# Kernel tuning notes

Measured on AMD Instinct MI355X. Metric: run time of the kernel, lower is better.

Reference implementation:

```python
import jax, jax.numpy as jnp
import numpy as np

B, LQ, D, H, L, P, DFF = 16, 1024, 256, 8, 4, 4, 1024
SHAPES = ((64, 64), (32, 32), (16, 16), (8, 8))  # (H_l, W_l) per level
LV = sum(h * w for h, w in SHAPES)  # 5440
DH = D // H
EPS = 1e-5


def layer_norm(x, g, b):
    m = jnp.mean(x, -1, keepdims=True)
    v = jnp.mean((x - m) ** 2, -1, keepdims=True)
    return (x - m) * jax.lax.rsqrt(v + EPS) * g + b


def mha(q_in, k_in, v_in, w, b, ow, ob):
    # torch nn.MultiheadAttention with packed in_proj [3D, D]
    q = (q_in @ w[:D].T + b[:D]).reshape(B, LQ, H, DH)
    k = (k_in @ w[D:2 * D].T + b[D:2 * D]).reshape(B, LQ, H, DH)
    v = (v_in @ w[2 * D:].T + b[2 * D:]).reshape(B, LQ, H, DH)
    a = jax.nn.softmax(jnp.einsum('bqhd,bkhd->bhqk', q, k) * (1.0 / np.sqrt(DH)), -1)
    o = jnp.einsum('bhqk,bkhd->bqhd', a, v).reshape(B, LQ, D)
    return o @ ow.T + ob


def ms_deform_attn(q, ref, src, value_w, value_b, off_w, off_b, attw_w, attw_b, outp_w, outp_b):
    # value: [B, H, LV, DH]
    value = (src @ value_w.T + value_b).reshape(B, LV, H, DH).transpose(0, 2, 1, 3)
    off = (q @ off_w.T + off_b).reshape(B, LQ, H, L, P, 2)
    attw = jax.nn.softmax((q @ attw_w.T + attw_b).reshape(B, LQ, H, L * P), -1).reshape(B, LQ, H, L, P)
    # offset normalizer = (W_l, H_l) matching (x, y) order of reference points
    normalizer = jnp.array([[w, h] for h, w in SHAPES], jnp.float32)
    loc = ref[:, :, None, :, None, :] + off / normalizer[None, None, None, :, None, :]  # [B,LQ,H,L,P,2]
    out = jnp.zeros((B, LQ, H, DH), jnp.float32)
    start = 0
    for l, (hl, wl) in enumerate(SHAPES):
        v = value[:, :, start:start + hl * wl]  # [B,H,N_l,DH]
        start += hl * wl
        # grid_sample semantics, align_corners=False, padding zeros
        x = loc[:, :, :, l, :, 0] * wl - 0.5  # [B,LQ,H,P]
        y = loc[:, :, :, l, :, 1] * hl - 0.5
        x0 = jnp.floor(x); y0 = jnp.floor(y)
        lx = (x - x0).transpose(0, 2, 1, 3)[..., None]  # [B,H,LQ,P,1]
        ly = (y - y0).transpose(0, 2, 1, 3)[..., None]
        x0i = x0.astype(jnp.int32); y0i = y0.astype(jnp.int32)

        def gather(xi, yi):
            valid = ((xi >= 0) & (xi < wl) & (yi >= 0) & (yi < hl)).astype(jnp.float32)
            idx = jnp.clip(yi, 0, hl - 1) * wl + jnp.clip(xi, 0, wl - 1)  # [B,LQ,H,P]
            idx2 = idx.transpose(0, 2, 1, 3).reshape(B, H, LQ * P)
            g = jnp.take_along_axis(v, jnp.broadcast_to(idx2[..., None], (B, H, LQ * P, DH)), axis=2)
            return g.reshape(B, H, LQ, P, DH) * valid.transpose(0, 2, 1, 3)[..., None]

        g00 = gather(x0i, y0i); g01 = gather(x0i + 1, y0i)
        g10 = gather(x0i, y0i + 1); g11 = gather(x0i + 1, y0i + 1)
        sampled = (g00 * (1 - lx) * (1 - ly) + g01 * lx * (1 - ly)
                   + g10 * (1 - lx) * ly + g11 * lx * ly)  # [B,H,LQ,P,DH]
        out = out + jnp.einsum('bhqpd,bqhp->bqhd', sampled, attw[:, :, :, l])
    return out.reshape(B, LQ, D) @ outp_w.T + outp_b


def setup_inputs() -> dict:
    key = jax.random.key(0)
    ks = jax.random.split(key, 16)
    s = 0.02
    inp = {}
    inp['tgt'] = jax.random.normal(ks[0], (B, LQ, D), jnp.float32)
    inp['query_pos'] = jax.random.normal(ks[1], (B, LQ, D), jnp.float32)
    inp['reference_points'] = jax.random.uniform(ks[2], (B, LQ, L, 2), jnp.float32)
    inp['src'] = jax.random.normal(ks[3], (B, LV, D), jnp.float32)
    # self-attention (MHA)
    inp['in_proj_w'] = jax.random.normal(ks[4], (3 * D, D), jnp.float32) * s
    inp['in_proj_b'] = jnp.zeros((3 * D,), jnp.float32)
    inp['out_proj_w'] = jax.random.normal(ks[5], (D, D), jnp.float32) * s
    inp['out_proj_b'] = jnp.zeros((D,), jnp.float32)
    inp['norm2_g'] = jnp.ones((D,), jnp.float32); inp['norm2_b'] = jnp.zeros((D,), jnp.float32)
    # MSDeformAttn
    inp['value_w'] = jax.random.normal(ks[6], (D, D), jnp.float32) * s
    inp['value_b'] = jnp.zeros((D,), jnp.float32)
    inp['off_w'] = jax.random.normal(ks[7], (H * L * P * 2, D), jnp.float32) * s
    inp['off_b'] = jax.random.normal(ks[8], (H * L * P * 2,), jnp.float32) * 0.5
    inp['attw_w'] = jax.random.normal(ks[9], (H * L * P, D), jnp.float32) * s
    inp['attw_b'] = jnp.zeros((H * L * P,), jnp.float32)
    inp['outp_w'] = jax.random.normal(ks[10], (D, D), jnp.float32) * s
    inp['outp_b'] = jnp.zeros((D,), jnp.float32)
    inp['norm1_g'] = jnp.ones((D,), jnp.float32); inp['norm1_b'] = jnp.zeros((D,), jnp.float32)
    # FFN
    inp['lin1_w'] = jax.random.normal(ks[11], (DFF, D), jnp.float32) * s
    inp['lin1_b'] = jnp.zeros((DFF,), jnp.float32)
    inp['lin2_w'] = jax.random.normal(ks[12], (D, DFF), jnp.float32) * s
    inp['lin2_b'] = jnp.zeros((D,), jnp.float32)
    inp['norm3_g'] = jnp.ones((D,), jnp.float32); inp['norm3_b'] = jnp.zeros((D,), jnp.float32)
    inp['src_spatial_shapes'] = jnp.array(SHAPES, jnp.int32)
    inp['level_start_index'] = jnp.array(np.concatenate([[0], np.cumsum([h * w for h, w in SHAPES[:-1]])]), jnp.int32)
    return inp


def reference(tgt, query_pos, reference_points, src,
              in_proj_w, in_proj_b, out_proj_w, out_proj_b, norm2_g, norm2_b,
              value_w, value_b, off_w, off_b, attw_w, attw_b, outp_w, outp_b,
              norm1_g, norm1_b, lin1_w, lin1_b, lin2_w, lin2_b, norm3_g, norm3_b,
              src_spatial_shapes, level_start_index):
    # dropout=0 (eval mode)
    q = tgt + query_pos
    tgt2 = mha(q, q, tgt, in_proj_w, in_proj_b, out_proj_w, out_proj_b)
    tgt = layer_norm(tgt + tgt2, norm2_g, norm2_b)
    tgt2 = ms_deform_attn(tgt + query_pos, reference_points, src,
                          value_w, value_b, off_w, off_b, attw_w, attw_b, outp_w, outp_b)
    tgt = layer_norm(tgt + tgt2, norm1_g, norm1_b)
    t2 = jax.nn.relu(tgt @ lin1_w.T + lin1_b) @ lin2_w.T + lin2_b
    return layer_norm(tgt + t2, norm3_g, norm3_b)
```

## Files before the change

### kernel.cpp

```cpp
#include <hip/hip_runtime.h>
#include <math.h>

typedef short s16x8 __attribute__((ext_vector_type(8)));
typedef float f32x4 __attribute__((ext_vector_type(4)));
typedef unsigned short u16;
typedef unsigned short u16x4 __attribute__((ext_vector_type(4)));

constexpr int cB    = 16;
constexpr int cLQ   = 1024;
constexpr int cD    = 256;
constexpr int cH    = 8;
constexpr int cLVTOT= 5440;
constexpr int cNTOK = cB * cLQ;
constexpr int cNV   = cB * cLVTOT;

__device__ __forceinline__ u16 f2b(float f) {
    __bf16 h = (__bf16)f;
    u16 u;
    __builtin_memcpy(&u, &h, 2);
    return u;
}
__device__ __forceinline__ float bl(unsigned x) {
    return __uint_as_float(x << 16);
}
__device__ __forceinline__ void load16(const u16* g, u16* l) {
    __builtin_amdgcn_global_load_lds((const __attribute__((address_space(1))) void*)g,
                                     (__attribute__((address_space(3))) void*)l, 16, 0, 0);
}

__global__ __launch_bounds__(256) void cvt_kernel(const float4* __restrict__ in,
                                                  u16x4* __restrict__ out) {
    int i = blockIdx.x * 256 + threadIdx.x;
    float4 v = in[i];
    out[i] = (u16x4){ f2b(v.x), f2b(v.y), f2b(v.z), f2b(v.w) };
}

struct WArgs { const float4* src[8]; };
__global__ __launch_bounds__(256) void cvtw_kernel(WArgs a, u16x4* __restrict__ out) {
    int i = blockIdx.x * 256 + threadIdx.x;
    int s, off;
    if (i < 98304) {
        if (i < 65536) { if (i < 49152) { s = 0; off = i; } else { s = 1; off = i - 49152; } }
        else           { if (i < 81920) { s = 2; off = i - 65536; } else { s = 3; off = i - 81920; } }
    } else {
        if (i < 122880){ if (i < 106496){ s = 4; off = i - 98304; } else { s = 5; off = i - 106496; } }
        else           { if (i < 188416){ s = 6; off = i - 122880; } else { s = 7; off = i - 188416; } }
    }
    float4 v = a.src[s][off];
    out[i] = (u16x4){ f2b(v.x), f2b(v.y), f2b(v.z), f2b(v.w) };
}

__global__ __launch_bounds__(256) void prep_kernel(const float4* __restrict__ t,
                                                   const float4* __restrict__ q,
                                                   u16x4* __restrict__ tb,
                                                   u16x4* __restrict__ qb) {
    int i = blockIdx.x * 256 + threadIdx.x;
    float4 a = t[i], b = q[i];
    tb[i] = (u16x4){ f2b(a.x), f2b(a.y), f2b(a.z), f2b(a.w) };
    qb[i] = (u16x4){ f2b(a.x + b.x), f2b(a.y + b.y), f2b(a.z + b.z), f2b(a.w + b.w) };
}

template <int RELU, int OUTBF>
__global__ __launch_bounds__(256) void gemm128(const u16* __restrict__ A,
                                               const u16* __restrict__ Wt,
                                               const float* __restrict__ bias,
                                               float* __restrict__ Cf,
                                               u16* __restrict__ Cb,
                                               int M, int N, int K) {
    __shared__ u16 As[128 * 32];
    __shared__ u16 Bs[128 * 32];
    int tid = threadIdx.x;
    int bm = blockIdx.x * 128, bn = blockIdx.y * 128;
    int w = tid >> 6, lane = tid & 63, quad = lane >> 4, l15 = lane & 15;
    int wm = (w & 1) * 64, wn = (w >> 1) * 64;
    int r0 = tid >> 2;
    int c0 = ((tid & 3) ^ ((tid >> 3) & 3)) * 8;
    const u16* ga0 = A  + (size_t)(bm + r0) * K + c0;
    const u16* ga1 = ga0 + (size_t)64 * K;
    const u16* gb0 = Wt + (size_t)(bn + r0) * K + c0;
    const u16* gb1 = gb0 + (size_t)64 * K;
    u16* la0 = As + (tid & 192) * 8;
    u16* la1 = As + 64 * 32 + (tid & 192) * 8;
    u16* lb0 = Bs + (tid & 192) * 8;
    u16* lb1 = Bs + 64 * 32 + (tid & 192) * 8;
    int abk = (quad ^ ((l15 >> 1) & 3)) * 8;
    f32x4 acc[16];
#pragma unroll
    for (int i = 0; i < 16; ++i) acc[i] = (f32x4){0.f, 0.f, 0.f, 0.f};
    for (int k0 = 0; k0 < K; k0 += 32) {
        __syncthreads();
        load16(ga0 + k0, la0);
        load16(ga1 + k0, la1);
        load16(gb0 + k0, lb0);
        load16(gb1 + k0, lb1);
        __syncthreads();
        s16x8 af[4], bf[4];
#pragma unroll
        for (int mt = 0; mt < 4; ++mt) af[mt] = *(const s16x8*)&As[(wm + mt * 16 + l15) * 32 + abk];
#pragma unroll
        for (int nt = 0; nt < 4; ++nt) bf[nt] = *(const s16x8*)&Bs[(wn + nt * 16 + l15) * 32 + abk];
#pragma unroll
        for (int mt = 0; mt < 4; ++mt)
#pragma unroll
            for (int nt = 0; nt < 4; ++nt)
                acc[mt * 4 + nt] = __builtin_amdgcn_mfma_f32_16x16x32_bf16(af[mt], bf[nt], acc[mt * 4 + nt], 0, 0, 0);
    }
    float bs[4];
#pragma unroll
    for (int nt = 0; nt < 4; ++nt) bs[nt] = bias[bn + wn + nt * 16 + l15];
#pragma unroll
    for (int mt = 0; mt < 4; ++mt) {
        int m = bm + wm + mt * 16 + quad * 4;
#pragma unroll
        for (int nt = 0; nt < 4; ++nt) {
            int n = bn + wn + nt * 16 + l15;
#pragma unroll
            for (int r = 0; r < 4; ++r) {
                float v = acc[mt * 4 + nt][r] + bs[nt];
                if (RELU) v = fmaxf(v, 0.f);
                if (OUTBF) Cb[(size_t)(m + r) * N + n] = f2b(v);
                else       Cf[(size_t)(m + r) * N + n] = v;
            }
        }
    }
}

template <int RELU, int OUTBF>
__global__ __launch_bounds__(256) void gemm64(const u16* __restrict__ A,
                                              const u16* __restrict__ Wt,
                                              const float* __restrict__ bias,
                                              float* __restrict__ Cf,
                                              u16* __restrict__ Cb,
                                              int M, int N, int K) {
    __shared__ u16 As[64 * 32];
    __shared__ u16 Bs[128 * 32];
    int tid = threadIdx.x;
    int bm = blockIdx.x * 64, bn = blockIdx.y * 128;
    int w = tid >> 6, lane = tid & 63, quad = lane >> 4, l15 = lane & 15;
    int wn = w * 32;
    int r0 = tid >> 2;
    int c0 = ((tid & 3) ^ ((tid >> 3) & 3)) * 8;
    const u16* ga0 = A  + (size_t)(bm + r0) * K + c0;
    const u16* gb0 = Wt + (size_t)(bn + r0) * K + c0;
    const u16* gb1 = gb0 + (size_t)64 * K;
    u16* la0 = As + (tid & 192) * 8;
    u16* lb0 = Bs + (tid & 192) * 8;
    u16* lb1 = Bs + 64 * 32 + (tid & 192) * 8;
    int abk = (quad ^ ((l15 >> 1) & 3)) * 8;
    f32x4 acc[8];
#pragma unroll
    for (int i = 0; i < 8; ++i) acc[i] = (f32x4){0.f, 0.f, 0.f, 0.f};
    for (int k0 = 0; k0 < K; k0 += 32) {
        __syncthreads();
        load16(ga0 + k0, la0);
        load16(gb0 + k0, lb0);
        load16(gb1 + k0, lb1);
        __syncthreads();
        s16x8 af[4], bf[2];
#pragma unroll
        for (int mt = 0; mt < 4; ++mt) af[mt] = *(const s16x8*)&As[(mt * 16 + l15) * 32 + abk];
#pragma unroll
        for (int nt = 0; nt < 2; ++nt) bf[nt] = *(const s16x8*)&Bs[(wn + nt * 16 + l15) * 32 + abk];
#pragma unroll
        for (int mt = 0; mt < 4; ++mt)
#pragma unroll
            for (int nt = 0; nt < 2; ++nt)
                acc[mt * 2 + nt] = __builtin_amdgcn_mfma_f32_16x16x32_bf16(af[mt], bf[nt], acc[mt * 2 + nt], 0, 0, 0);
    }
    float bs[2];
#pragma unroll
    for (int nt = 0; nt < 2; ++nt) bs[nt] = bias[bn + wn + nt * 16 + l15];
#pragma unroll
    for (int mt = 0; mt < 4; ++mt) {
        int m = bm + mt * 16 + quad * 4;
#pragma unroll
        for (int nt = 0; nt < 2; ++nt) {
            int n = bn + wn + nt * 16 + l15;
#pragma unroll
            for (int r = 0; r < 4; ++r) {
                float v = acc[mt * 2 + nt][r] + bs[nt];
                if (RELU) v = fmaxf(v, 0.f);
                if (OUTBF) Cb[(size_t)(m + r) * N + n] = f2b(v);
                else       Cf[(size_t)(m + r) * N + n] = v;
            }
        }
    }
}

__global__ __launch_bounds__(256) void vtrans_kernel(const u16* __restrict__ Vb,
                                                     u16* __restrict__ Vtg) {
    __shared__ u16 T[64 * 40];
    int tid = threadIdx.x;
    int tt = blockIdx.x & 15, bh = blockIdx.x >> 4;
    int h = bh & 7, b = bh >> 3;
    int r = tid >> 2, c = (tid & 3) * 8;
    *(s16x8*)&T[r * 40 + c] =
        *(const s16x8*)(Vb + (size_t)(b * cLQ + tt * 64 + r) * cD + h * 32 + c);
    __syncthreads();
    int dh = tid & 31, tc = (tid >> 5) * 8;
    s16x8 o;
#pragma unroll
    for (int i = 0; i < 8; ++i) o[i] = T[(tc + i) * 40 + dh];
    *(s16x8*)(Vtg + ((size_t)bh * 32 + dh) * cLQ + tt * 64 + tc) = o;
}

__global__ __launch_bounds__(256) void attn_mfma(const u16* __restrict__ QK,
                                                 const u16* __restrict__ Vt,
                                                 u16* __restrict__ O) {
    __shared__ u16 Ks[64 * 40];
    __shared__ u16 Vs[32 * 88];
    __shared__ u16 Ps[4][16 * 88];
    int tid = threadIdx.x, w = tid >> 6, lane = tid & 63, quad = lane >> 4, l15 = lane & 15;
    int qt = blockIdx.x & 15, bh = blockIdx.x >> 4;
    int h = bh & 7, b = bh >> 3;
    int qbase = qt * 64 + w * 16;
    const float C = 0.25506734f;
    s16x8 qf = *(const s16x8*)(QK + (size_t)(b * cLQ + qbase + l15) * 512 + h * 32 + quad * 8);
    f32x4 o0 = {0.f,0.f,0.f,0.f}, o1 = {0.f,0.f,0.f,0.f};
    float lsum = 0.f;
    int skey = tid >> 2, sdh = (tid & 3) * 8;
    int vdh = tid >> 3, vkc = (tid & 7) * 8;
    size_t kgbase = (size_t)(b * cLQ) * 512 + 256 + h * 32;
    size_t vgbase = (size_t)bh * 32 * cLQ;
    for (int kt = 0; kt < cLQ; kt += 64) {
        __syncthreads();
        *(s16x8*)&Ks[skey * 40 + sdh] = *(const s16x8*)(QK + kgbase + (size_t)(kt + skey) * 512 + sdh);
        *(s16x8*)&Vs[vdh * 88 + vkc]  = *(const s16x8*)(Vt + vgbase + (size_t)vdh * cLQ + kt + vkc);
        __syncthreads();
#pragma unroll
        for (int t = 0; t < 4; ++t) {
            s16x8 kf = *(const s16x8*)&Ks[(t * 16 + l15) * 40 + quad * 8];
            f32x4 z = {0.f,0.f,0.f,0.f};
            f32x4 sc = __builtin_amdgcn_mfma_f32_16x16x32_bf16(kf, qf, z, 0, 0, 0);
            u16x4 pb;
#pragma unroll
            for (int r = 0; r < 4; ++r) {
                float p = exp2f(sc[r] * C);
                lsum += p;
                pb[r] = f2b(p);
            }
            *(u16x4*)&Ps[w][l15 * 88 + t * 16 + quad * 4] = pb;
        }
#pragma unroll
        for (int ks = 0; ks < 2; ++ks) {
            s16x8 pa  = *(const s16x8*)&Ps[w][l15 * 88 + ks * 32 + quad * 8];
            s16x8 vb0 = *(const s16x8*)&Vs[l15 * 88 + ks * 32 + quad * 8];
            s16x8 vb1 = *(const s16x8*)&Vs[(l15 + 16) * 88 + ks * 32 + quad * 8];
            o0 = __builtin_amdgcn_mfma_f32_16x16x32_bf16(pa, vb0, o0, 0, 0, 0);
            o1 = __builtin_amdgcn_mfma_f32_16x16x32_bf16(pa, vb1, o1, 0, 0, 0);
        }
    }
    lsum += __shfl_xor(lsum, 16);
    lsum += __shfl_xor(lsum, 32);
#pragma unroll
    for (int r = 0; r < 4; ++r) {
        float inv = 1.0f / __shfl(lsum, quad * 4 + r);
        int q = qbase + quad * 4 + r;
        size_t ob = (size_t)(b * cLQ + q) * cD + h * 32;
        O[ob + l15]      = f2b(o0[r] * inv);
        O[ob + 16 + l15] = f2b(o1[r] * inv);
    }
}

template <int WB, int QP>
__global__ __launch_bounds__(256) void add_ln_kernel(const float* __restrict__ X,
                                                     const float* __restrict__ R,
                                                     const float* __restrict__ g,
                                                     const float* __restrict__ bt,
                                                     const float* __restrict__ qp,
                                                     float* __restrict__ out,
                                                     u16* __restrict__ outb) {
    int wave = threadIdx.x / 64;
    int lane = threadIdx.x % 64;
    int row = blockIdx.x * 4 + wave;
    const float* x = X + (size_t)row * cD;
    const float* r = R + (size_t)row * cD;
    float4 xv = *(const float4*)(x + lane * 4);
    float4 rv = *(const float4*)(r + lane * 4);
    float v0 = xv.x + rv.x, v1 = xv.y + rv.y, v2 = xv.z + rv.z, v3 = xv.w + rv.w;
    float s = v0 + v1 + v2 + v3;
    float s2 = v0 * v0 + v1 * v1 + v2 * v2 + v3 * v3;
#pragma unroll
    for (int off = 32; off > 0; off >>= 1) {
        s += __shfl_xor(s, off);
        s2 += __shfl_xor(s2, off);
    }
    float mean = s * (1.0f / 256.0f);
    float var = s2 * (1.0f / 256.0f) - mean * mean;
    float rstd = rsqrtf(var + 1e-5f);
    float4 gv = *(const float4*)(g + lane * 4);
    float4 bv = *(const float4*)(bt + lane * 4);
    float4 o;
    o.x = (v0 - mean) * rstd * gv.x + bv.x;
    o.y = (v1 - mean) * rstd * gv.y + bv.y;
    o.z = (v2 - mean) * rstd * gv.z + bv.z;
    o.w = (v3 - mean) * rstd * gv.w + bv.w;
    *(float4*)(out + (size_t)row * cD + lane * 4) = o;
    if (WB) {
        u16x4 ob = { f2b(o.x), f2b(o.y), f2b(o.z), f2b(o.w) };
        *(u16x4*)(outb + (size_t)row * cD + lane * 4) = ob;
    }
    if (QP) {
        float4 qv = *(const float4*)(qp + (size_t)row * cD + lane * 4);
        u16x4 ob = { f2b(o.x + qv.x), f2b(o.y + qv.y), f2b(o.z + qv.z), f2b(o.w + qv.w) };
        *(u16x4*)(outb + (size_t)row * cD + lane * 4) = ob;
    }
}

__global__ __launch_bounds__(256) void deform_kernel(const u16* __restrict__ value,
                                                     const float* __restrict__ oa,
                                                     const float* __restrict__ refp,
                                                     u16* __restrict__ out) {
    int t = blockIdx.x * 32 + (threadIdx.x >> 3);
    int dq = threadIdx.x & 7;
    int h = t & 7;
    int bq = t >> 3;
    int b = bq >> 10;
    const float* al = oa + (size_t)bq * 384 + 256 + h * 16;
    float wv[16];
    float mx = -1e30f;
#pragma unroll
    for (int i = 0; i < 16; ++i) { wv[i] = al[i]; mx = fmaxf(mx, wv[i]); }
    float sum = 0.f;
#pragma unroll
    for (int i = 0; i < 16; ++i) { wv[i] = __expf(wv[i] - mx); sum += wv[i]; }
    float inv = 1.f / sum;
    const float* off = oa + (size_t)bq * 384 + h * 32;
    const float* rp = refp + (size_t)bq * 8;
    const u16* vb = value + ((size_t)b * cLVTOT) * 256 + h * 32 + dq * 4;
    const int starts[4] = {0, 4096, 5120, 5376};
    const int dims[4] = {64, 32, 16, 8};
    float a0 = 0.f, a1 = 0.f, a2 = 0.f, a3 = 0.f;
#pragma unroll
    for (int l = 0; l < 4; ++l) {
        int hl = dims[l], wl = dims[l];
        float rx = rp[l * 2 + 0], ry = rp[l * 2 + 1];
#pragma unroll
        for (int p = 0; p < 4; ++p) {
            float ox = off[(l * 4 + p) * 2 + 0];
            float oy = off[(l * 4 + p) * 2 + 1];
            float x = rx * (float)wl + ox - 0.5f;
            float y = ry * (float)hl + oy - 0.5f;
            float x0f = floorf(x), y0f = floorf(y);
            float lx = x - x0f, ly = y - y0f;
            int x0 = (int)x0f, y0 = (int)y0f;
            float aw = wv[l * 4 + p] * inv;
            float cw[4] = {(1.f - lx) * (1.f - ly), lx * (1.f - ly),
                           (1.f - lx) * ly, lx * ly};
            int xs[4] = {x0, x0 + 1, x0, x0 + 1};
            int ys[4] = {y0, y0, y0 + 1, y0 + 1};
#pragma unroll
            for (int c = 0; c < 4; ++c) {
                int xi = xs[c], yi = ys[c];
                bool valid = (xi >= 0) && (xi < wl) && (yi >= 0) && (yi < hl);
                int xc = min(max(xi, 0), wl - 1);
                int yc = min(max(yi, 0), hl - 1);
                int idx = starts[l] + yc * wl + xc;
                float wgt = valid ? aw * cw[c] : 0.f;
                unsigned long long u = *(const unsigned long long*)(vb + (size_t)idx * 256);
                a0 += wgt * bl((unsigned)(u & 0xffffull));
                a1 += wgt * bl((unsigned)((u >> 16) & 0xffffull));
                a2 += wgt * bl((unsigned)((u >> 32) & 0xffffull));
                a3 += wgt * bl((unsigned)(u >> 48));
            }
        }
    }
    u16x4 o = { f2b(a0), f2b(a1), f2b(a2), f2b(a3) };
    *(u16x4*)(out + (size_t)bq * 256 + h * 32 + dq * 4) = o;
}

extern "C" void kernel_launch(void* const* d_in, const int* in_sizes, int n_in,
                              void* d_out, int out_size, void* d_ws, size_t ws_size,
                              hipStream_t stream) {
    const float* tgt        = (const float*)d_in[0];
    const float* query_pos  = (const float*)d_in[1];
    const float* refp       = (const float*)d_in[2];
    const float* src        = (const float*)d_in[3];
    const float* in_proj_w  = (const float*)d_in[4];
    const float* in_proj_b  = (const float*)d_in[5];
    const float* out_proj_w = (const float*)d_in[6];
    const float* out_proj_b = (const float*)d_in[7];
    const float* norm2_g    = (const float*)d_in[8];
    const float* norm2_b    = (const float*)d_in[9];
    const float* value_w    = (const float*)d_in[10];
    const float* value_b    = (const float*)d_in[11];
    const float* off_w      = (const float*)d_in[12];
    const float* off_b      = (const float*)d_in[13];
    const float* attw_w     = (const float*)d_in[14];
    const float* attw_b     = (const float*)d_in[15];
    const float* outp_w     = (const float*)d_in[16];
    const float* outp_b     = (const float*)d_in[17];
    const float* norm1_g    = (const float*)d_in[18];
    const float* norm1_b    = (const float*)d_in[19];
    const float* lin1_w     = (const float*)d_in[20];
    const float* lin1_b     = (const float*)d_in[21];
    const float* lin2_w     = (const float*)d_in[22];
    const float* lin2_b     = (const float*)d_in[23];
    const float* norm3_g    = (const float*)d_in[24];
    const float* norm3_b    = (const float*)d_in[25];

    char* W = (char*)d_ws;
    const size_t S84 = 8388608;
    u16*   tgtb  = (u16*)(W + 0);
    u16*   q2b   = (u16*)(W + 0);
    u16*   qb    = (u16*)(W + 1 * S84);
    u16*   QKb   = (u16*)(W + 2 * S84);
    u16*   dtb   = (u16*)(W + 2 * S84);
    u16*   x2b   = (u16*)(W + 3 * S84);
    u16*   Vb    = (u16*)(W + 4 * S84);
    float* ffn2f = (float*)(W + 4 * S84);
    u16*   aob   = (u16*)(W + 5 * S84);
    float* oaf   = (float*)(W + 5 * S84);
    u16*   Vtg   = (u16*)(W + 6 * S84);
    float* t2f   = (float*)(W + 6 * S84);
    float* x1f   = (float*)(W + 8 * S84);
    float* x2f   = (float*)(W + 10 * S84);
    u16*   srcb  = (u16*)(W + 12 * S84);
    u16*   ffn1b = (u16*)(W + 12 * S84);
    u16*   valb  = (u16*)(W + 12 * S84 + 44564480);
    char*  wbase = W + 12 * S84 + 2 * 44564480;
    u16* wb_in   = (u16*)(wbase + 0);
    u16* wb_out  = (u16*)(wbase + 393216);
    u16* wb_val  = (u16*)(wbase + 524288);
    u16* wb_off  = (u16*)(wbase + 655360);
    u16* wb_outp = (u16*)(wbase + 851968);
    u16* wb_lin1 = (u16*)(wbase + 983040);
    u16* wb_lin2 = (u16*)(wbase + 1507328);
    float* biasoa= (float*)(wbase + 2031616);
    float* out = (float*)d_out;

    dim3 blk(256);

    hipMemcpyAsync(biasoa,       off_b,  256 * 4, hipMemcpyDeviceToDevice, stream);
    hipMemcpyAsync(biasoa + 256, attw_b, 128 * 4, hipMemcpyDeviceToDevice, stream);

    prep_kernel<<<dim3(4096), blk, 0, stream>>>((const float4*)tgt, (const float4*)query_pos,
                                                (u16x4*)tgtb, (u16x4*)qb);
    WArgs wa;
    wa.src[0] = (const float4*)in_proj_w;  wa.src[1] = (const float4*)out_proj_w;
    wa.src[2] = (const float4*)value_w;    wa.src[3] = (const float4*)off_w;
    wa.src[4] = (const float4*)attw_w;     wa.src[5] = (const float4*)outp_w;
    wa.src[6] = (const float4*)lin1_w;     wa.src[7] = (const float4*)lin2_w;
    cvtw_kernel<<<dim3(992), blk, 0, stream>>>(wa, (u16x4*)wb_in);
    cvt_kernel<<<dim3(21760), blk, 0, stream>>>((const float4*)src, (u16x4*)srcb);

    gemm128<0, 1><<<dim3(128, 4), blk, 0, stream>>>(qb,   wb_in,             in_proj_b,       nullptr, QKb, cNTOK, 512, 256);
    gemm64 <0, 1><<<dim3(256, 2), blk, 0, stream>>>(tgtb, wb_in + 512 * 256, in_proj_b + 512, nullptr, Vb,  cNTOK, 256, 256);
    vtrans_kernel<<<dim3(2048), blk, 0, stream>>>(Vb, Vtg);
    attn_mfma<<<dim3(cB * cH * 16), blk, 0, stream>>>(QKb, Vtg, aob);
    gemm64 <0, 0><<<dim3(256, 2), blk, 0, stream>>>(aob, wb_out, out_proj_b, t2f, nullptr, cNTOK, 256, 256);
    add_ln_kernel<0, 1><<<dim3(4096), blk, 0, stream>>>(tgt, t2f, norm2_g, norm2_b, query_pos, x1f, q2b);

    gemm128<0, 1><<<dim3(680, 2), blk, 0, stream>>>(srcb, wb_val, value_b, nullptr, valb, cNV, 256, 256);
    gemm64 <0, 0><<<dim3(256, 3), blk, 0, stream>>>(q2b, wb_off, biasoa, oaf, nullptr, cNTOK, 384, 256);
    deform_kernel<<<dim3(4096), blk, 0, stream>>>(valb, oaf, refp, dtb);
    gemm64 <0, 0><<<dim3(256, 2), blk, 0, stream>>>(dtb, wb_outp, outp_b, t2f, nullptr, cNTOK, 256, 256);
    add_ln_kernel<1, 0><<<dim3(4096), blk, 0, stream>>>(x1f, t2f, norm1_g, norm1_b, nullptr, x2f, x2b);

    gemm128<1, 1><<<dim3(128, 8), blk, 0, stream>>>(x2b, wb_lin1, lin1_b, nullptr, ffn1b, cNTOK, 1024, 256);
    gemm64 <0, 0><<<dim3(256, 2), blk, 0, stream>>>(ffn1b, wb_lin2, lin2_b, ffn2f, nullptr, cNTOK, 256, 1024);
    add_ln_kernel<0, 0><<<dim3(4096), blk, 0, stream>>>(x2f, ffn2f, norm3_g, norm3_b, nullptr, out, nullptr);
}
```

Baseline: 473.8 us.

## Double-buffer GEMM LDS tiles, fuse QKV projection with V transpose, prefetch attention tiles

Both GEMM kernels now use two LDS buffers, so the next K-slice is loaded while MFMAs run on the current one. A new gemm_qkv kernel computes Q, K and V in one launch and writes V directly in transposed per-head layout, which removes the separate V GEMM and the vtrans kernel. The attention kernel prefetches the next K/V tile into registers and shrinks the LDS row padding from 88 to 72. The cost is twice the shared memory per GEMM block, which may lower occupancy, plus possible bank-conflict changes from the new padding.

```diff
diff --git a/kernel.cpp b/kernel.cpp
--- a/kernel.cpp
+++ b/kernel.cpp
@@ -60,6 +60,91 @@
     qb[i] = (u16x4){ f2b(a.x + b.x), f2b(a.y + b.y), f2b(a.z + b.z), f2b(a.w + b.w) };
 }
 
+__global__ __launch_bounds__(256) void gemm_qkv(const u16* __restrict__ A0,
+                                                const u16* __restrict__ A1,
+                                                const u16* __restrict__ Wt,
+                                                const float* __restrict__ bias,
+                                                u16* __restrict__ QKb,
+                                                u16* __restrict__ Vtg) {
+    __shared__ u16 As[2][128 * 32];
+    __shared__ u16 Bs[2][128 * 32];
+    const int K = 256;
+    int tid = threadIdx.x;
+    int bm = blockIdx.x * 128, bn = blockIdx.y * 128;
+    const u16* A = (blockIdx.y < 4) ? A0 : A1;
+    int w = tid >> 6, lane = tid & 63, quad = lane >> 4, l15 = lane & 15;
+    int wm = (w & 1) * 64, wn = (w >> 1) * 64;
+    int r0 = tid >> 2;
+    int c0 = ((tid & 3) ^ ((tid >> 3) & 3)) * 8;
+    const u16* ga0 = A  + (size_t)(bm + r0) * K + c0;
+    const u16* ga1 = ga0 + (size_t)64 * K;
+    const u16* gb0 = Wt + (size_t)(bn + r0) * K + c0;
+    const u16* gb1 = gb0 + (size_t)64 * K;
+    int lofs = (tid & 192) * 8;
+    int abk = (quad ^ ((l15 >> 1) & 3)) * 8;
+    f32x4 acc[16];
+#pragma unroll
+    for (int i = 0; i < 16; ++i) acc[i] = (f32x4){0.f, 0.f, 0.f, 0.f};
+    load16(ga0, &As[0][lofs]);
+    load16(ga1, &As[0][2048 + lofs]);
+    load16(gb0, &Bs[0][lofs]);
+    load16(gb1, &Bs[0][2048 + lofs]);
+#pragma unroll 2
+    for (int i = 0; i < 8; ++i) {
+        int cur = i & 1, nxt = cur ^ 1;
+        int k1 = (i + 1) << 5;
+        if (i < 7) {
+            load16(ga0 + k1, &As[nxt][lofs]);
+            load16(ga1 + k1, &As[nxt][2048 + lofs]);
+            load16(gb0 + k1, &Bs[nxt][lofs]);
+            load16(gb1 + k1, &Bs[nxt][2048 + lofs]);
+        }
+        __syncthreads();
+        s16x8 af[4], bf[4];
+#pragma unroll
+        for (int mt = 0; mt < 4; ++mt) af[mt] = *(const s16x8*)&As[cur][(wm + mt * 16 + l15) * 32 + abk];
+#pragma unroll
+        for (int nt = 0; nt < 4; ++nt) bf[nt] = *(const s16x8*)&Bs[cur][(wn + nt * 16 + l15) * 32 + abk];
+#pragma unroll
+        for (int mt = 0; mt < 4; ++mt)
+#pragma unroll
+            for (int nt = 0; nt < 4; ++nt)
+                acc[mt * 4 + nt] = __builtin_amdgcn_mfma_f32_16x16x32_bf16(af[mt], bf[nt], acc[mt * 4 + nt], 0, 0, 0);
+        __syncthreads();
+    }
+    float bs[4];
+#pragma unroll
+    for (int nt = 0; nt < 4; ++nt) bs[nt] = bias[bn + wn + nt * 16 + l15];
+    if (bn < 512) {
+#pragma unroll
+        for (int mt = 0; mt < 4; ++mt) {
+            int m = bm + wm + mt * 16 + quad * 4;
+#pragma unroll
+            for (int nt = 0; nt < 4; ++nt) {
+                int n = bn + wn + nt * 16 + l15;
+#pragma unroll
+                for (int r = 0; r < 4; ++r)
+                    QKb[(size_t)(m + r) * 512 + n] = f2b(acc[mt * 4 + nt][r] + bs[nt]);
+            }
+        }
+    } else {
+#pragma unroll
+        for (int mt = 0; mt < 4; ++mt) {
+            int m = bm + wm + mt * 16 + quad * 4;
+            int b = m >> 10, t = m & 1023;
+#pragma unroll
+            for (int nt = 0; nt < 4; ++nt) {
+                int nv = bn + wn + nt * 16 + l15 - 512;
+                int h = nv >> 5, dh = nv & 31;
+                u16x4 o;
+#pragma unroll
+                for (int r = 0; r < 4; ++r) o[r] = f2b(acc[mt * 4 + nt][r] + bs[nt]);
+                *(u16x4*)(Vtg + (((size_t)(b * 8 + h) * 32 + dh) << 10) + t) = o;
+            }
+        }
+    }
+}
+
 template <int RELU, int OUTBF>
 __global__ __launch_bounds__(256) void gemm128(const u16* __restrict__ A,
                                                const u16* __restrict__ Wt,
@@ -67,8 +152,8 @@
                                                float* __restrict__ Cf,
                                                u16* __restrict__ Cb,
                                                int M, int N, int K) {
-    __shared__ u16 As[128 * 32];
-    __shared__ u16 Bs[128 * 32];
+    __shared__ u16 As[2][128 * 32];
+    __shared__ u16 Bs[2][128 * 32];
     int tid = threadIdx.x;
     int bm = blockIdx.x * 128, bn = blockIdx.y * 128;
     int w = tid >> 6, lane = tid & 63, quad = lane >> 4, l15 = lane & 15;
@@ -79,31 +164,38 @@
     const u16* ga1 = ga0 + (size_t)64 * K;
     const u16* gb0 = Wt + (size_t)(bn + r0) * K + c0;
     const u16* gb1 = gb0 + (size_t)64 * K;
-    u16* la0 = As + (tid & 192) * 8;
-    u16* la1 = As + 64 * 32 + (tid & 192) * 8;
-    u16* lb0 = Bs + (tid & 192) * 8;
-    u16* lb1 = Bs + 64 * 32 + (tid & 192) * 8;
+    int lofs = (tid & 192) * 8;
     int abk = (quad ^ ((l15 >> 1) & 3)) * 8;
     f32x4 acc[16];
 #pragma unroll
     for (int i = 0; i < 16; ++i) acc[i] = (f32x4){0.f, 0.f, 0.f, 0.f};
-    for (int k0 = 0; k0 < K; k0 += 32) {
-        __syncthreads();
-        load16(ga0 + k0, la0);
-        load16(ga1 + k0, la1);
-        load16(gb0 + k0, lb0);
-        load16(gb1 + k0, lb1);
+    load16(ga0, &As[0][lofs]);
+    load16(ga1, &As[0][2048 + lofs]);
+    load16(gb0, &Bs[0][lofs]);
+    load16(gb1, &Bs[0][2048 + lofs]);
+    int nk = K >> 5;
+#pragma unroll 2
+    for (int i = 0; i < nk; ++i) {
+        int cur = i & 1, nxt = cur ^ 1;
+        int k1 = (i + 1) << 5;
+        if (i + 1 < nk) {
+            load16(ga0 + k1, &As[nxt][lofs]);
+            load16(ga1 + k1, &As[nxt][2048 + lofs]);
+            load16(gb0 + k1, &Bs[nxt][lofs]);
+            load16(gb1 + k1, &Bs[nxt][2048 + lofs]);
+        }
         __syncthreads();
         s16x8 af[4], bf[4];
 #pragma unroll
-        for (int mt = 0; mt < 4; ++mt) af[mt] = *(const s16x8*)&As[(wm + mt * 16 + l15) * 32 + abk];
-#pragma unroll
-        for (int nt = 0; nt < 4; ++nt) bf[nt] = *(const s16x8*)&Bs[(wn + nt * 16 + l15) * 32 + abk];
+        for (int mt = 0; mt < 4; ++mt) af[mt] = *(const s16x8*)&As[cur][(wm + mt * 16 + l15) * 32 + abk];
+#pragma unroll
+        for (int nt = 0; nt < 4; ++nt) bf[nt] = *(const s16x8*)&Bs[cur][(wn + nt * 16 + l15) * 32 + abk];
 #pragma unroll
         for (int mt = 0; mt < 4; ++mt)
 #pragma unroll
             for (int nt = 0; nt < 4; ++nt)
                 acc[mt * 4 + nt] = __builtin_amdgcn_mfma_f32_16x16x32_bf16(af[mt], bf[nt], acc[mt * 4 + nt], 0, 0, 0);
+        __syncthreads();
     }
     float bs[4];
 #pragma unroll
@@ -132,8 +224,8 @@
                                               float* __restrict__ Cf,
                                               u16* __restrict__ Cb,
                                               int M, int N, int K) {
-    __shared__ u16 As[64 * 32];
-    __shared__ u16 Bs[128 * 32];
+    __shared__ u16 As[2][64 * 32];
+    __shared__ u16 Bs[2][128 * 32];
     int tid = threadIdx.x;
     int bm = blockIdx.x * 64, bn = blockIdx.y * 128;
     int w = tid >> 6, lane = tid & 63, quad = lane >> 4, l15 = lane & 15;
@@ -143,29 +235,36 @@
     const u16* ga0 = A  + (size_t)(bm + r0) * K + c0;
     const u16* gb0 = Wt + (size_t)(bn + r0) * K + c0;
     const u16* gb1 = gb0 + (size_t)64 * K;
-    u16* la0 = As + (tid & 192) * 8;
-    u16* lb0 = Bs + (tid & 192) * 8;
-    u16* lb1 = Bs + 64 * 32 + (tid & 192) * 8;
+    int lofs = (tid & 192) * 8;
     int abk = (quad ^ ((l15 >> 1) & 3)) * 8;
     f32x4 acc[8];
 #pragma unroll
     for (int i = 0; i < 8; ++i) acc[i] = (f32x4){0.f, 0.f, 0.f, 0.f};
-    for (int k0 = 0; k0 < K; k0 += 32) {
-        __syncthreads();
-        load16(ga0 + k0, la0);
-        load16(gb0 + k0, lb0);
-        load16(gb1 + k0, lb1);
+    load16(ga0, &As[0][lofs]);
+    load16(gb0, &Bs[0][lofs]);
+    load16(gb1, &Bs[0][2048 + lofs]);
+    int nk = K >> 5;
+#pragma unroll 2
+    for (int i = 0; i < nk; ++i) {
+        int cur = i & 1, nxt = cur ^ 1;
+        int k1 = (i + 1) << 5;
+        if (i + 1 < nk) {
+            load16(ga0 + k1, &As[nxt][lofs]);
+            load16(gb0 + k1, &Bs[nxt][lofs]);
+            load16(gb1 + k1, &Bs[nxt][2048 + lofs]);
+        }
         __syncthreads();
         s16x8 af[4], bf[2];
 #pragma unroll
-        for (int mt = 0; mt < 4; ++mt) af[mt] = *(const s16x8*)&As[(mt * 16 + l15) * 32 + abk];
-#pragma unroll
-        for (int nt = 0; nt < 2; ++nt) bf[nt] = *(const s16x8*)&Bs[(wn + nt * 16 + l15) * 32 + abk];
+        for (int mt = 0; mt < 4; ++mt) af[mt] = *(const s16x8*)&As[cur][(mt * 16 + l15) * 32 + abk];
+#pragma unroll
+        for (int nt = 0; nt < 2; ++nt) bf[nt] = *(const s16x8*)&Bs[cur][(wn + nt * 16 + l15) * 32 + abk];
 #pragma unroll
         for (int mt = 0; mt < 4; ++mt)
 #pragma unroll
             for (int nt = 0; nt < 2; ++nt)
                 acc[mt * 2 + nt] = __builtin_amdgcn_mfma_f32_16x16x32_bf16(af[mt], bf[nt], acc[mt * 2 + nt], 0, 0, 0);
+        __syncthreads();
     }
     float bs[2];
 #pragma unroll
@@ -187,29 +286,12 @@
     }
 }
 
-__global__ __launch_bounds__(256) void vtrans_kernel(const u16* __restrict__ Vb,
-                                                     u16* __restrict__ Vtg) {
-    __shared__ u16 T[64 * 40];
-    int tid = threadIdx.x;
-    int tt = blockIdx.x & 15, bh = blockIdx.x >> 4;
-    int h = bh & 7, b = bh >> 3;
-    int r = tid >> 2, c = (tid & 3) * 8;
-    *(s16x8*)&T[r * 40 + c] =
-        *(const s16x8*)(Vb + (size_t)(b * cLQ + tt * 64 + r) * cD + h * 32 + c);
-    __syncthreads();
-    int dh = tid & 31, tc = (tid >> 5) * 8;
-    s16x8 o;
-#pragma unroll
-    for (int i = 0; i < 8; ++i) o[i] = T[(tc + i) * 40 + dh];
-    *(s16x8*)(Vtg + ((size_t)bh * 32 + dh) * cLQ + tt * 64 + tc) = o;
-}
-
 __global__ __launch_bounds__(256) void attn_mfma(const u16* __restrict__ QK,
                                                  const u16* __restrict__ Vt,
                                                  u16* __restrict__ O) {
     __shared__ u16 Ks[64 * 40];
-    __shared__ u16 Vs[32 * 88];
-    __shared__ u16 Ps[4][16 * 88];
+    __shared__ u16 Vs[32 * 72];
+    __shared__ u16 Ps[4][16 * 72];
     int tid = threadIdx.x, w = tid >> 6, lane = tid & 63, quad = lane >> 4, l15 = lane & 15;
     int qt = blockIdx.x & 15, bh = blockIdx.x >> 4;
     int h = bh & 7, b = bh >> 3;
@@ -222,10 +304,16 @@
     int vdh = tid >> 3, vkc = (tid & 7) * 8;
     size_t kgbase = (size_t)(b * cLQ) * 512 + 256 + h * 32;
     size_t vgbase = (size_t)bh * 32 * cLQ;
+    s16x8 kreg = *(const s16x8*)(QK + kgbase + (size_t)skey * 512 + sdh);
+    s16x8 vreg = *(const s16x8*)(Vt + vgbase + (size_t)vdh * cLQ + vkc);
     for (int kt = 0; kt < cLQ; kt += 64) {
         __syncthreads();
-        *(s16x8*)&Ks[skey * 40 + sdh] = *(const s16x8*)(QK + kgbase + (size_t)(kt + skey) * 512 + sdh);
-        *(s16x8*)&Vs[vdh * 88 + vkc]  = *(const s16x8*)(Vt + vgbase + (size_t)vdh * cLQ + kt + vkc);
+        *(s16x8*)&Ks[skey * 40 + sdh] = kreg;
+        *(s16x8*)&Vs[vdh * 72 + vkc]  = vreg;
+        if (kt + 64 < cLQ) {
+            kreg = *(const s16x8*)(QK + kgbase + (size_t)(kt + 64 + skey) * 512 + sdh);
+            vreg = *(const s16x8*)(Vt + vgbase + (size_t)vdh * cLQ + kt + 64 + vkc);
+        }
         __syncthreads();
 #pragma unroll
         for (int t = 0; t < 4; ++t) {
@@ -239,13 +327,13 @@
                 lsum += p;
                 pb[r] = f2b(p);
             }
-            *(u16x4*)&Ps[w][l15 * 88 + t * 16 + quad * 4] = pb;
+            *(u16x4*)&Ps[w][l15 * 72 + t * 16 + quad * 4] = pb;
         }
 #pragma unroll
         for (int ks = 0; ks < 2; ++ks) {
-            s16x8 pa  = *(const s16x8*)&Ps[w][l15 * 88 + ks * 32 + quad * 8];
-            s16x8 vb0 = *(const s16x8*)&Vs[l15 * 88 + ks * 32 + quad * 8];
-            s16x8 vb1 = *(const s16x8*)&Vs[(l15 + 16) * 88 + ks * 32 + quad * 8];
+            s16x8 pa  = *(const s16x8*)&Ps[w][l15 * 72 + ks * 32 + quad * 8];
+            s16x8 vb0 = *(const s16x8*)&Vs[l15 * 72 + ks * 32 + quad * 8];
+            s16x8 vb1 = *(const s16x8*)&Vs[(l15 + 16) * 72 + ks * 32 + quad * 8];
             o0 = __builtin_amdgcn_mfma_f32_16x16x32_bf16(pa, vb0, o0, 0, 0, 0);
             o1 = __builtin_amdgcn_mfma_f32_16x16x32_bf16(pa, vb1, o1, 0, 0, 0);
         }
@@ -384,17 +472,12 @@
     const float* norm2_b    = (const float*)d_in[9];
     const float* value_w    = (const float*)d_in[10];
     const float* value_b    = (const float*)d_in[11];
-    const float* off_w      = (const float*)d_in[12];
     const float* off_b      = (const float*)d_in[13];
-    const float* attw_w     = (const float*)d_in[14];
     const float* attw_b     = (const float*)d_in[15];
-    const float* outp_w     = (const float*)d_in[16];
     const float* outp_b     = (const float*)d_in[17];
     const float* norm1_g    = (const float*)d_in[18];
     const float* norm1_b    = (const float*)d_in[19];
-    const float* lin1_w     = (const float*)d_in[20];
     const float* lin1_b     = (const float*)d_in[21];
-    const float* lin2_w     = (const float*)d_in[22];
     const float* lin2_b     = (const float*)d_in[23];
     const float* norm3_g    = (const float*)d_in[24];
     const float* norm3_b    = (const float*)d_in[25];
@@ -407,7 +490,6 @@
     u16*   QKb   = (u16*)(W + 2 * S84);
     u16*   dtb   = (u16*)(W + 2 * S84);
     u16*   x2b   = (u16*)(W + 3 * S84);
-    u16*   Vb    = (u16*)(W + 4 * S84);
     float* ffn2f = (float*)(W + 4 * S84);
     u16*   aob   = (u16*)(W + 5 * S84);
     float* oaf   = (float*)(W + 5 * S84);
@@ -438,26 +520,24 @@
                                                 (u16x4*)tgtb, (u16x4*)qb);
     WArgs wa;
     wa.src[0] = (const float4*)in_proj_w;  wa.src[1] = (const float4*)out_proj_w;
-    wa.src[2] = (const float4*)value_w;    wa.src[3] = (const float4*)off_w;
-    wa.src[4] = (const float4*)attw_w;     wa.src[5] = (const float4*)outp_w;
-    wa.src[6] = (const float4*)lin1_w;     wa.src[7] = (const float4*)lin2_w;
+    wa.src[2] = (const float4*)value_w;    wa.src[3] = (const float4*)d_in[12];
+    wa.src[4] = (const float4*)d_in[14];   wa.src[5] = (const float4*)d_in[16];
+    wa.src[6] = (const float4*)d_in[20];   wa.src[7] = (const float4*)d_in[22];
     cvtw_kernel<<<dim3(992), blk, 0, stream>>>(wa, (u16x4*)wb_in);
     cvt_kernel<<<dim3(21760), blk, 0, stream>>>((const float4*)src, (u16x4*)srcb);
 
-    gemm128<0, 1><<<dim3(128, 4), blk, 0, stream>>>(qb,   wb_in,             in_proj_b,       nullptr, QKb, cNTOK, 512, 256);
-    gemm64 <0, 1><<<dim3(256, 2), blk, 0, stream>>>(tgtb, wb_in + 512 * 256, in_proj_b + 512, nullptr, Vb,  cNTOK, 256, 256);
-    vtrans_kernel<<<dim3(2048), blk, 0, stream>>>(Vb, Vtg);
+    gemm_qkv<<<dim3(128, 6), blk, 0, stream>>>(qb, tgtb, wb_in, in_proj_b, QKb, Vtg);
     attn_mfma<<<dim3(cB * cH * 16), blk, 0, stream>>>(QKb, Vtg, aob);
-    gemm64 <0, 0><<<dim3(256, 2), blk, 0, stream>>>(aob, wb_out, out_proj_b, t2f, nullptr, cNTOK, 256, 256);
+    gemm64<0, 0><<<dim3(256, 2), blk, 0, stream>>>(aob, wb_out, out_proj_b, t2f, nullptr, cNTOK, 256, 256);
     add_ln_kernel<0, 1><<<dim3(4096), blk, 0, stream>>>(tgt, t2f, norm2_g, norm2_b, query_pos, x1f, q2b);
 
     gemm128<0, 1><<<dim3(680, 2), blk, 0, stream>>>(srcb, wb_val, value_b, nullptr, valb, cNV, 256, 256);
-    gemm64 <0, 0><<<dim3(256, 3), blk, 0, stream>>>(q2b, wb_off, biasoa, oaf, nullptr, cNTOK, 384, 256);
+    gemm64<0, 0><<<dim3(256, 3), blk, 0, stream>>>(q2b, wb_off, biasoa, oaf, nullptr, cNTOK, 384, 256);
     deform_kernel<<<dim3(4096), blk, 0, stream>>>(valb, oaf, refp, dtb);
-    gemm64 <0, 0><<<dim3(256, 2), blk, 0, stream>>>(dtb, wb_outp, outp_b, t2f, nullptr, cNTOK, 256, 256);
+    gemm64<0, 0><<<dim3(256, 2), blk, 0, stream>>>(dtb, wb_outp, outp_b, t2f, nullptr, cNTOK, 256, 256);
     add_ln_kernel<1, 0><<<dim3(4096), blk, 0, stream>>>(x1f, t2f, norm1_g, norm1_b, nullptr, x2f, x2b);
 
     gemm128<1, 1><<<dim3(128, 8), blk, 0, stream>>>(x2b, wb_lin1, lin1_b, nullptr, ffn1b, cNTOK, 1024, 256);
-    gemm64 <0, 0><<<dim3(256, 2), blk, 0, stream>>>(ffn1b, wb_lin2, lin2_b, ffn2f, nullptr, cNTOK, 256, 1024);
+    gemm64<0, 0><<<dim3(256, 2), blk, 0, stream>>>(ffn1b, wb_lin2, lin2_b, ffn2f, nullptr, cNTOK, 256, 1024);
     add_ln_kernel<0, 0><<<dim3(4096), blk, 0, stream>>>(x2f, ffn2f, norm3_g, norm3_b, nullptr, out, nullptr);
 }
```

New measurement: 458.0 us. 3.3% less time.
